# Kernel tuning notes

Hardware: AMD Instinct MI355X
Metric: run time of the kernel (lower is better)

Reference implementation:

```python
import jax, jax.numpy as jnp
import numpy as np
import math

ORDER = 7
VAR_SIZE = ORDER + 1
ROW_SIZE = 2048
BATCH = 2048
DIM = 64
COL_SIZE = 16384


def setup_inputs() -> dict:
    key = jax.random.key(0)
    k0, k1, k2, k3, k4, k5, k6 = jax.random.split(key, 7)
    events = jax.random.randint(k0, (ROW_SIZE, BATCH), 0, 2, dtype=jnp.int32)
    col_indices = jax.random.randint(k1, (BATCH,), 0, COL_SIZE, dtype=jnp.int32)
    col_times = jax.random.uniform(k2, (BATCH,), dtype=jnp.float32)
    z_rows = jax.random.uniform(k3, (VAR_SIZE, ROW_SIZE, DIM), dtype=jnp.float32)
    z_cols = jax.random.uniform(k4, (COL_SIZE, DIM), dtype=jnp.float32)
    gamma_rows = jax.random.uniform(k5, (ROW_SIZE,), dtype=jnp.float32)
    gamma_cols = jax.random.uniform(k6, (COL_SIZE,), dtype=jnp.float32)
    return {"events": events, "col_indices": col_indices, "col_times": col_times,
            "z_rows": z_rows, "z_cols": z_cols,
            "gamma_rows": gamma_rows, "gamma_cols": gamma_cols}


def reference(events, col_indices, col_times, z_rows, z_cols, gamma_rows, gamma_cols):
    O = z_rows.shape[0]  # var_size = order + 1
    inv_fact = jnp.asarray([1.0 / math.factorial(o) for o in range(O)], dtype=z_rows.dtype)
    # T[o, b] = t_b^o / o!  (Taylor basis per column time)
    tpow = jnp.power(col_times[None, :], jnp.arange(O, dtype=col_times.dtype)[:, None]) * inv_fact[:, None]
    # Time-varying row positions: z_t[b, n, d] = sum_o z_rows[o, n, d] * T[o, b]
    z_t = jnp.einsum('ond,ob->bnd', z_rows, tpow)
    # Pairwise L2 distance to the matched column embedding (cdist with a single col per time)
    diff = z_t - z_cols[col_indices][:, None, :]            # [B, N, D]
    dist = jnp.sqrt(jnp.sum(diff * diff, axis=-1))          # [B, N]
    logits = gamma_rows[None, :] + gamma_cols[col_indices][:, None] - dist  # [B, N]
    p = jax.nn.sigmoid(logits)
    e = events.T.astype(p.dtype)                            # [B, N]
    # p_mat = p if event else (1 - p)
    p_mat = 1.0 - e - (1.0 - 2.0 * e) * p
    return -jnp.sum(jnp.log(p_mat))
```

## Files before the change

### kernel.cpp

```cpp
#include <hip/hip_runtime.h>
#include <math.h>
#include <stdint.h>

#define NR    2048
#define NB    2048
#define DIMD  64
#define KC    576
#define KSTEP 18

typedef __bf16 bf16x8 __attribute__((ext_vector_type(8)));
typedef float  f32x4  __attribute__((ext_vector_type(4)));

typedef const __attribute__((address_space(1))) void* gas_p;
typedef __attribute__((address_space(3))) void*       las_p;

__device__ __forceinline__ unsigned short f2bf(float f) {
    unsigned int u = __float_as_uint(f);
    unsigned int r = u + 0x7FFFu + ((u >> 16) & 1u);
    return (unsigned short)(r >> 16);
}

__global__ __launch_bounds__(256) void prep_a(
    const int*   __restrict__ col_indices,
    const float* __restrict__ col_times,
    const float* __restrict__ z_cols,
    const float* __restrict__ gamma_cols,
    unsigned short* __restrict__ Abuf,
    float* __restrict__ cc, float* __restrict__ gcg)
{
    __shared__ float Tl[4][8];
    const int tid = threadIdx.x, w = tid >> 6, lane = tid & 63;
    const int b  = blockIdx.x * 4 + w;
    const float t  = col_times[b];
    const int   ci = col_indices[b];
    if (lane < 8) {
        float v = 1.f;
        for (int i = 1; i <= lane; ++i) v = v * t / (float)i;
        Tl[w][lane] = v;
    }
    __syncthreads();
    const float cd = z_cols[ci * DIMD + lane];
    unsigned short* arow = Abuf + (size_t)b * KC;
#pragma unroll
    for (int o = 0; o < 8; ++o)
        arow[o * 64 + lane] = f2bf(-2.f * Tl[w][o] * cd);
    arow[512 + lane] = f2bf(Tl[w][lane >> 3] * Tl[w][lane & 7]);
    float s = cd * cd;
#pragma unroll
    for (int m = 1; m < 64; m <<= 1) s += __shfl_xor(s, m, 64);
    if (lane == 0) { cc[b] = s; gcg[b] = gamma_cols[ci]; }
}

__global__ __launch_bounds__(256) void prep_b(
    const float* __restrict__ z_rows,
    unsigned short* __restrict__ Bbuf)
{
    const int tid = threadIdx.x, w = tid >> 6, lane = tid & 63;
    const int n = blockIdx.x * 4 + w;
    float z8[8];
#pragma unroll
    for (int o = 0; o < 8; ++o)
        z8[o] = z_rows[o * (NR * DIMD) + n * DIMD + lane];
    unsigned short* brow = Bbuf + (size_t)n * KC;
#pragma unroll
    for (int o = 0; o < 8; ++o)
        brow[o * 64 + lane] = f2bf(z8[o]);
    float myG = 0.f;
#pragma unroll
    for (int o1 = 0; o1 < 8; ++o1)
#pragma unroll
        for (int o2 = o1; o2 < 8; ++o2) {
            float p = z8[o1] * z8[o2];
#pragma unroll
            for (int m = 1; m < 64; m <<= 1) p += __shfl_xor(p, m, 64);
            if (lane == o1 * 8 + o2) myG = p;
            if (o1 != o2 && lane == o2 * 8 + o1) myG = p;
        }
    brow[512 + lane] = f2bf(myG);
}

__global__ __launch_bounds__(256, 2) void p2v_gemm(
    const unsigned short* __restrict__ Abuf,
    const unsigned short* __restrict__ Bbuf,
    const float* __restrict__ cc,
    const float* __restrict__ gcg,
    const float* __restrict__ gamma_rows,
    const int*   __restrict__ events,
    float*       __restrict__ out)
{
    __shared__ unsigned short As[128 * 32] __attribute__((aligned(16)));
    __shared__ unsigned short Bs[64 * 32]  __attribute__((aligned(16)));
    __shared__ float warr[4];

    const int tid = threadIdx.x, w = tid >> 6, lane = tid & 63;
    const int wm = w >> 1, wn = w & 1;
    const int n0 = blockIdx.x * 64, b0 = blockIdx.y * 128;

    const int lr = lane >> 2, lsl = lane & 3;
    const size_t gA0 = (size_t)(b0 + w * 32 + lr) * KC + lsl * 8;
    const size_t gA1 = gA0 + (size_t)16 * KC;
    const size_t gB0 = (size_t)(n0 + w * 16 + lr) * KC + lsl * 8;
    unsigned short* dstA0 = &As[(w * 32) * 32];
    unsigned short* dstA1 = &As[(w * 32 + 16) * 32];
    unsigned short* dstB0 = &Bs[(w * 16) * 32];

    f32x4 acc[4][2];
#pragma unroll
    for (int mi = 0; mi < 4; ++mi)
#pragma unroll
        for (int ni = 0; ni < 2; ++ni) acc[mi][ni] = (f32x4)(0.f);

    for (int ks = 0; ks < KSTEP; ++ks) {
        const int ko = ks * 32;
        __builtin_amdgcn_global_load_lds((gas_p)(Abuf + gA0 + ko), (las_p)dstA0, 16, 0, 0);
        __builtin_amdgcn_global_load_lds((gas_p)(Abuf + gA1 + ko), (las_p)dstA1, 16, 0, 0);
        __builtin_amdgcn_global_load_lds((gas_p)(Bbuf + gB0 + ko), (las_p)dstB0, 16, 0, 0);
        __syncthreads();
        bf16x8 af[4], bfr[2];
#pragma unroll
        for (int mi = 0; mi < 4; ++mi)
            af[mi] = *reinterpret_cast<const bf16x8*>(
                &As[(wm * 64 + mi * 16 + (lane & 15)) * 32 + (lane >> 4) * 8]);
#pragma unroll
        for (int ni = 0; ni < 2; ++ni)
            bfr[ni] = *reinterpret_cast<const bf16x8*>(
                &Bs[(wn * 32 + ni * 16 + (lane & 15)) * 32 + (lane >> 4) * 8]);
#pragma unroll
        for (int mi = 0; mi < 4; ++mi)
#pragma unroll
            for (int ni = 0; ni < 2; ++ni)
                acc[mi][ni] = __builtin_amdgcn_mfma_f32_16x16x32_bf16(
                    af[mi], bfr[ni], acc[mi][ni], 0, 0, 0);
        __syncthreads();
    }

    float ls = 0.f;
#pragma unroll
    for (int ni = 0; ni < 2; ++ni) {
        const int n = n0 + wn * 32 + ni * 16 + (lane & 15);
        const float grn = gamma_rows[n];
        const size_t erow = (size_t)n * NB;
#pragma unroll
        for (int mi = 0; mi < 4; ++mi) {
            const int bb = b0 + wm * 64 + mi * 16 + (lane >> 4) * 4;
            const int4   ev  = *reinterpret_cast<const int4*>(&events[erow + bb]);
            const float4 ccv = *reinterpret_cast<const float4*>(&cc[bb]);
            const float4 gcv = *reinterpret_cast<const float4*>(&gcg[bb]);
#define EPJ(cmp, evv)                                                      \
            {                                                              \
                const float d2   = acc[mi][ni].cmp + ccv.cmp;              \
                const float dist = sqrtf(fmaxf(d2, 0.f));                  \
                const float L    = grn + gcv.cmp - dist;                   \
                const float x    = (evv != 0) ? -L : L;                    \
                ls += fmaxf(x, 0.f) + __logf(1.f + __expf(-fabsf(x)));     \
            }
            EPJ(x, ev.x) EPJ(y, ev.y) EPJ(z, ev.z) EPJ(w, ev.w)
#undef EPJ
        }
    }
#pragma unroll
    for (int m = 1; m < 64; m <<= 1) ls += __shfl_xor(ls, m, 64);
    if (lane == 0) warr[w] = ls;
    __syncthreads();
    if (tid == 0) atomicAdd(out, warr[0] + warr[1] + warr[2] + warr[3]);
}

extern "C" void kernel_launch(void* const* d_in, const int* in_sizes, int n_in,
                              void* d_out, int out_size, void* d_ws, size_t ws_size,
                              hipStream_t stream) {
    const int*   events      = (const int*)  d_in[0];
    const int*   col_indices = (const int*)  d_in[1];
    const float* col_times   = (const float*)d_in[2];
    const float* z_rows      = (const float*)d_in[3];
    const float* z_cols      = (const float*)d_in[4];
    const float* gamma_rows  = (const float*)d_in[5];
    const float* gamma_cols  = (const float*)d_in[6];
    float*       out         = (float*)d_out;

    unsigned short* Abuf = (unsigned short*)d_ws;
    unsigned short* Bbuf = Abuf + (size_t)NB * KC;
    float*          cc   = (float*)(Bbuf + (size_t)NR * KC);
    float*          gcg  = cc + NB;

    hipMemsetAsync(out, 0, sizeof(float) * out_size, stream);
    prep_a<<<NB / 4, 256, 0, stream>>>(col_indices, col_times, z_cols, gamma_cols,
                                       Abuf, cc, gcg);
    prep_b<<<NR / 4, 256, 0, stream>>>(z_rows, Bbuf);
    dim3 grid(NR / 64, NB / 128);
    p2v_gemm<<<grid, 256, 0, stream>>>(Abuf, Bbuf, cc, gcg, gamma_rows, events, out);
}
```

Before: 106.4 us.

## Merge prep kernels, double GEMM K-tile to 64 with XOR-swizzled LDS

Combines the two preprocessing kernels into a single launch that splits on block index, saving one kernel launch. The GEMM K-tile grows from 32 to 64, halving the number of sync-bracketed load iterations. Each LDS row is XOR-swizzled by row index so the 16-byte fragment reads avoid bank conflicts. The cost is twice the LDS per block and more in-flight loads per step, with no double buffering.

```diff
diff --git a/kernel.cpp b/kernel.cpp
--- a/kernel.cpp
+++ b/kernel.cpp
@@ -6,7 +6,8 @@
 #define NB    2048
 #define DIMD  64
 #define KC    576
-#define KSTEP 18
+#define BK    64
+#define KSTEP 9
 
 typedef __bf16 bf16x8 __attribute__((ext_vector_type(8)));
 typedef float  f32x4  __attribute__((ext_vector_type(4)));
@@ -20,63 +21,61 @@
     return (unsigned short)(r >> 16);
 }
 
-__global__ __launch_bounds__(256) void prep_a(
+__global__ __launch_bounds__(256) void prep_all(
     const int*   __restrict__ col_indices,
     const float* __restrict__ col_times,
     const float* __restrict__ z_cols,
     const float* __restrict__ gamma_cols,
+    const float* __restrict__ z_rows,
     unsigned short* __restrict__ Abuf,
+    unsigned short* __restrict__ Bbuf,
     float* __restrict__ cc, float* __restrict__ gcg)
 {
-    __shared__ float Tl[4][8];
     const int tid = threadIdx.x, w = tid >> 6, lane = tid & 63;
-    const int b  = blockIdx.x * 4 + w;
-    const float t  = col_times[b];
-    const int   ci = col_indices[b];
-    if (lane < 8) {
-        float v = 1.f;
-        for (int i = 1; i <= lane; ++i) v = v * t / (float)i;
-        Tl[w][lane] = v;
+    if (blockIdx.x < 512) {
+        __shared__ float Tl[4][8];
+        const int b  = blockIdx.x * 4 + w;
+        const float t  = col_times[b];
+        const int   ci = col_indices[b];
+        if (lane < 8) {
+            float v = 1.f;
+            for (int i = 1; i <= lane; ++i) v = v * t / (float)i;
+            Tl[w][lane] = v;
+        }
+        __syncthreads();
+        const float cd = z_cols[ci * DIMD + lane];
+        unsigned short* arow = Abuf + (size_t)b * KC;
+#pragma unroll
+        for (int o = 0; o < 8; ++o)
+            arow[o * 64 + lane] = f2bf(-2.f * Tl[w][o] * cd);
+        arow[512 + lane] = f2bf(Tl[w][lane >> 3] * Tl[w][lane & 7]);
+        float s = cd * cd;
+#pragma unroll
+        for (int m = 1; m < 64; m <<= 1) s += __shfl_xor(s, m, 64);
+        if (lane == 0) { cc[b] = s; gcg[b] = gamma_cols[ci]; }
+    } else {
+        const int n = (blockIdx.x - 512) * 4 + w;
+        float z8[8];
+#pragma unroll
+        for (int o = 0; o < 8; ++o)
+            z8[o] = z_rows[o * (NR * DIMD) + n * DIMD + lane];
+        unsigned short* brow = Bbuf + (size_t)n * KC;
+#pragma unroll
+        for (int o = 0; o < 8; ++o)
+            brow[o * 64 + lane] = f2bf(z8[o]);
+        float myG = 0.f;
+#pragma unroll
+        for (int o1 = 0; o1 < 8; ++o1)
+#pragma unroll
+            for (int o2 = o1; o2 < 8; ++o2) {
+                float p = z8[o1] * z8[o2];
+#pragma unroll
+                for (int m = 1; m < 64; m <<= 1) p += __shfl_xor(p, m, 64);
+                if (lane == o1 * 8 + o2) myG = p;
+                if (o1 != o2 && lane == o2 * 8 + o1) myG = p;
+            }
+        brow[512 + lane] = f2bf(myG);
     }
-    __syncthreads();
-    const float cd = z_cols[ci * DIMD + lane];
-    unsigned short* arow = Abuf + (size_t)b * KC;
-#pragma unroll
-    for (int o = 0; o < 8; ++o)
-        arow[o * 64 + lane] = f2bf(-2.f * Tl[w][o] * cd);
-    arow[512 + lane] = f2bf(Tl[w][lane >> 3] * Tl[w][lane & 7]);
-    float s = cd * cd;
-#pragma unroll
-    for (int m = 1; m < 64; m <<= 1) s += __shfl_xor(s, m, 64);
-    if (lane == 0) { cc[b] = s; gcg[b] = gamma_cols[ci]; }
-}
-
-__global__ __launch_bounds__(256) void prep_b(
-    const float* __restrict__ z_rows,
-    unsigned short* __restrict__ Bbuf)
-{
-    const int tid = threadIdx.x, w = tid >> 6, lane = tid & 63;
-    const int n = blockIdx.x * 4 + w;
-    float z8[8];
-#pragma unroll
-    for (int o = 0; o < 8; ++o)
-        z8[o] = z_rows[o * (NR * DIMD) + n * DIMD + lane];
-    unsigned short* brow = Bbuf + (size_t)n * KC;
-#pragma unroll
-    for (int o = 0; o < 8; ++o)
-        brow[o * 64 + lane] = f2bf(z8[o]);
-    float myG = 0.f;
-#pragma unroll
-    for (int o1 = 0; o1 < 8; ++o1)
-#pragma unroll
-        for (int o2 = o1; o2 < 8; ++o2) {
-            float p = z8[o1] * z8[o2];
-#pragma unroll
-            for (int m = 1; m < 64; m <<= 1) p += __shfl_xor(p, m, 64);
-            if (lane == o1 * 8 + o2) myG = p;
-            if (o1 != o2 && lane == o2 * 8 + o1) myG = p;
-        }
-    brow[512 + lane] = f2bf(myG);
 }
 
 __global__ __launch_bounds__(256, 2) void p2v_gemm(
@@ -88,21 +87,20 @@
     const int*   __restrict__ events,
     float*       __restrict__ out)
 {
-    __shared__ unsigned short As[128 * 32] __attribute__((aligned(16)));
-    __shared__ unsigned short Bs[64 * 32]  __attribute__((aligned(16)));
+    __shared__ unsigned short As[128 * BK] __attribute__((aligned(16)));
+    __shared__ unsigned short Bs[64 * BK]  __attribute__((aligned(16)));
     __shared__ float warr[4];
 
     const int tid = threadIdx.x, w = tid >> 6, lane = tid & 63;
     const int wm = w >> 1, wn = w & 1;
     const int n0 = blockIdx.x * 64, b0 = blockIdx.y * 128;
 
-    const int lr = lane >> 2, lsl = lane & 3;
-    const size_t gA0 = (size_t)(b0 + w * 32 + lr) * KC + lsl * 8;
-    const size_t gA1 = gA0 + (size_t)16 * KC;
-    const size_t gB0 = (size_t)(n0 + w * 16 + lr) * KC + lsl * 8;
-    unsigned short* dstA0 = &As[(w * 32) * 32];
-    unsigned short* dstA1 = &As[(w * 32 + 16) * 32];
-    unsigned short* dstB0 = &Bs[(w * 16) * 32];
+    const int lr8 = lane >> 3;
+    const int cx  = (lane & 7) ^ lr8;
+    const size_t gA = (size_t)(b0 + w * 32 + lr8) * KC + cx * 8;
+    const size_t gB = (size_t)(n0 + w * 16 + lr8) * KC + cx * 8;
+    unsigned short* dA = &As[(w * 32) * BK];
+    unsigned short* dB = &Bs[(w * 16) * BK];
 
     f32x4 acc[4][2];
 #pragma unroll
@@ -111,26 +109,35 @@
         for (int ni = 0; ni < 2; ++ni) acc[mi][ni] = (f32x4)(0.f);
 
     for (int ks = 0; ks < KSTEP; ++ks) {
-        const int ko = ks * 32;
-        __builtin_amdgcn_global_load_lds((gas_p)(Abuf + gA0 + ko), (las_p)dstA0, 16, 0, 0);
-        __builtin_amdgcn_global_load_lds((gas_p)(Abuf + gA1 + ko), (las_p)dstA1, 16, 0, 0);
-        __builtin_amdgcn_global_load_lds((gas_p)(Bbuf + gB0 + ko), (las_p)dstB0, 16, 0, 0);
+        const int ko = ks * BK;
+#pragma unroll
+        for (int i = 0; i < 4; ++i)
+            __builtin_amdgcn_global_load_lds((gas_p)(Abuf + gA + (size_t)(i * 8) * KC + ko),
+                                             (las_p)(dA + i * 512), 16, 0, 0);
+#pragma unroll
+        for (int i = 0; i < 2; ++i)
+            __builtin_amdgcn_global_load_lds((gas_p)(Bbuf + gB + (size_t)(i * 8) * KC + ko),
+                                             (las_p)(dB + i * 512), 16, 0, 0);
         __syncthreads();
-        bf16x8 af[4], bfr[2];
 #pragma unroll
-        for (int mi = 0; mi < 4; ++mi)
-            af[mi] = *reinterpret_cast<const bf16x8*>(
-                &As[(wm * 64 + mi * 16 + (lane & 15)) * 32 + (lane >> 4) * 8]);
+        for (int kk = 0; kk < 2; ++kk) {
+            const int slot = (kk * 4 + (lane >> 4)) ^ (lane & 7);
+            bf16x8 af[4], bfr[2];
 #pragma unroll
-        for (int ni = 0; ni < 2; ++ni)
-            bfr[ni] = *reinterpret_cast<const bf16x8*>(
-                &Bs[(wn * 32 + ni * 16 + (lane & 15)) * 32 + (lane >> 4) * 8]);
-#pragma unroll
-        for (int mi = 0; mi < 4; ++mi)
+            for (int mi = 0; mi < 4; ++mi)
+                af[mi] = *reinterpret_cast<const bf16x8*>(
+                    &As[(wm * 64 + mi * 16 + (lane & 15)) * BK + slot * 8]);
 #pragma unroll
             for (int ni = 0; ni < 2; ++ni)
-                acc[mi][ni] = __builtin_amdgcn_mfma_f32_16x16x32_bf16(
-                    af[mi], bfr[ni], acc[mi][ni], 0, 0, 0);
+                bfr[ni] = *reinterpret_cast<const bf16x8*>(
+                    &Bs[(wn * 32 + ni * 16 + (lane & 15)) * BK + slot * 8]);
+#pragma unroll
+            for (int mi = 0; mi < 4; ++mi)
+#pragma unroll
+                for (int ni = 0; ni < 2; ++ni)
+                    acc[mi][ni] = __builtin_amdgcn_mfma_f32_16x16x32_bf16(
+                        af[mi], bfr[ni], acc[mi][ni], 0, 0, 0);
+        }
         __syncthreads();
     }
 
@@ -183,9 +190,8 @@
     float*          gcg  = cc + NB;
 
     hipMemsetAsync(out, 0, sizeof(float) * out_size, stream);
-    prep_a<<<NB / 4, 256, 0, stream>>>(col_indices, col_times, z_cols, gamma_cols,
-                                       Abuf, cc, gcg);
-    prep_b<<<NR / 4, 256, 0, stream>>>(z_rows, Bbuf);
+    prep_all<<<1024, 256, 0, stream>>>(col_indices, col_times, z_cols, gamma_cols,
+                                       z_rows, Abuf, Bbuf, cc, gcg);
     dim3 grid(NR / 64, NB / 128);
     p2v_gemm<<<grid, 256, 0, stream>>>(Abuf, Bbuf, cc, gcg, gamma_rows, events, out);
 }
```

Result: faster. 100.2 us (-5.8%).
